# Performance work log

Measured on AMD Instinct MI355X. Metric: run time of the kernel, lower is better.

## Reference

```python
import jax, jax.numpy as jnp
import numpy as np

N, E, D = 100000, 640000, 128

def setup_inputs() -> dict:
    key = jax.random.key(0)
    ks = jax.random.split(key, 12)
    s = 1.0 / np.sqrt(D)
    sg = 1.0 / np.sqrt(2 * D)
    return {
        "nodes": jax.random.normal(ks[0], (N, D), jnp.float32),
        "globals_": jax.random.normal(ks[1], (1, D), jnp.float32),
        "senders": jax.random.randint(ks[2], (E,), 0, N, jnp.int32),
        "receivers": jax.random.randint(ks[3], (E,), 0, N, jnp.int32),
        "W1_w": jax.random.normal(ks[4], (D, D), jnp.float32) * s,
        "W1_b": jnp.zeros((D,), jnp.float32),
        "W2_w": jax.random.normal(ks[5], (D, D), jnp.float32) * s,
        "W2_b": jnp.zeros((D,), jnp.float32),
        "W3_w": jax.random.normal(ks[6], (D, D), jnp.float32) * s,
        "W3_b": jnp.zeros((D,), jnp.float32),
        "Wg_w": jax.random.normal(ks[7], (2 * D, D), jnp.float32) * sg,
        "Wg_b": jnp.zeros((D,), jnp.float32),
    }


def reference(nodes, globals_, senders, receivers,
              W1_w, W1_b, W2_w, W2_b, W3_w, W3_b, Wg_w, Wg_b):
    n = nodes.shape[0]
    # W1 skip-branch projection
    h = nodes @ W1_w + W1_b                              # [N, D]
    # GraphConvolution: W2 projection + symmetric-normalized sum aggregation
    conv = nodes @ W2_w + W2_b                           # [N, D]
    ones = jnp.ones(senders.shape, conv.dtype)
    send_deg = jax.ops.segment_sum(ones, senders, num_segments=n)
    recv_deg = jax.ops.segment_sum(ones, receivers, num_segments=n)
    conv = conv * jax.lax.rsqrt(jnp.maximum(send_deg, 1.0))[:, None]
    agg = jax.ops.segment_sum(conv[senders], receivers, num_segments=n)  # gather + scatter
    agg = agg * jax.lax.rsqrt(jnp.maximum(recv_deg, 1.0))[:, None]
    h = h + agg
    # global -> node broadcast (globals is not None)
    h = h + (globals_[0:1] @ W3_w + W3_b)
    h = jax.nn.relu(h)
    h = h + nodes                                        # residual
    # global update: aggregate nodes (sum over single graph) + gated residual
    an = jnp.sum(h, axis=0, keepdims=True)               # [1, D]
    g_new = globals_ + jax.nn.relu(jnp.concatenate([an, globals_], axis=-1) @ Wg_w + Wg_b)
    return h, g_new
```

## Files before the change

kernel.cpp:

```cpp
#include <hip/hip_runtime.h>

#define D 128
#define SCH 1024

typedef __attribute__((ext_vector_type(8))) short short8;
typedef __attribute__((ext_vector_type(4))) float floatx4;

__device__ inline void bf16split(float x, ushort& hi, ushort& lo) {
  unsigned u = __float_as_uint(x);
  unsigned rh = (u + 0x7FFFu + ((u >> 16) & 1u)) & 0xFFFF0000u;
  hi = (ushort)(rh >> 16);
  float fl = x - __uint_as_float(rh);
  unsigned ul = __float_as_uint(fl);
  lo = (ushort)((ul + 0x7FFFu + ((ul >> 16) & 1u)) >> 16);
}

__global__ void k_gproj(const float* __restrict__ g, const float* __restrict__ W3,
                        const float* __restrict__ b3, float* __restrict__ gvec,
                        float* __restrict__ an) {
  if (blockIdx.x == 1) {
    if (threadIdx.x < D) an[threadIdx.x] = 0.f;
    return;
  }
  __shared__ float part[256];
  const int j = threadIdx.x & 127, half = threadIdx.x >> 7;
  float acc = 0.f;
  for (int k = half * 64; k < half * 64 + 64; ++k)
    acc = fmaf(g[k], W3[k * D + j], acc);
  part[threadIdx.x] = acc;
  __syncthreads();
  if (threadIdx.x < D) gvec[j] = b3[j] + part[j] + part[j + 128];
}

__global__ void k_degrees(const int* __restrict__ snd, const int* __restrict__ rcv,
                          int* __restrict__ cs, int* __restrict__ cr, int E) {
  const int e = blockIdx.x * blockDim.x + threadIdx.x;
  if (e < E) {
    atomicAdd(cs + snd[e], 1);
    atomicAdd(cr + rcv[e], 1);
  }
}

__global__ void k_scanA(const int* __restrict__ cnt, int* __restrict__ bsum, int n) {
  __shared__ int red[4];
  const int t = threadIdx.x;
  const int base = blockIdx.x * SCH + t * 4;
  int4 v = make_int4(0, 0, 0, 0);
  if (base < n) v = *(const int4*)(cnt + base);
  int s = v.x + v.y + v.z + v.w;
#pragma unroll
  for (int o = 32; o > 0; o >>= 1) s += __shfl_down(s, o, 64);
  if ((t & 63) == 0) red[t >> 6] = s;
  __syncthreads();
  if (t == 0) bsum[blockIdx.x] = red[0] + red[1] + red[2] + red[3];
}

__global__ void k_scanB(const int* __restrict__ bsum, int* __restrict__ bbase, int nb) {
  __shared__ int sh[256];
  const int t = threadIdx.x;
  const int v = (t < nb) ? bsum[t] : 0;
  sh[t] = v;
  __syncthreads();
  for (int st = 1; st < 256; st <<= 1) {
    const int u = (t >= st) ? sh[t - st] : 0;
    __syncthreads();
    sh[t] += u;
    __syncthreads();
  }
  if (t < nb) bbase[t] = sh[t] - v;
}

__global__ void k_scanC(const int* __restrict__ cnt, const int* __restrict__ bbase,
                        int* __restrict__ off, int* __restrict__ cursor, int n) {
  __shared__ int sh[256];
  const int t = threadIdx.x;
  const int base = blockIdx.x * SCH + t * 4;
  int4 v = make_int4(0, 0, 0, 0);
  if (base < n) v = *(const int4*)(cnt + base);
  const int s = v.x + v.y + v.z + v.w;
  sh[t] = s;
  __syncthreads();
  for (int st = 1; st < 256; st <<= 1) {
    const int u = (t >= st) ? sh[t - st] : 0;
    __syncthreads();
    sh[t] += u;
    __syncthreads();
  }
  const int ex = sh[t] - s + bbase[blockIdx.x];
  if (base < n) {
    const int4 o = make_int4(ex, ex + v.x, ex + v.x + v.y, ex + v.x + v.y + v.z);
    *(int4*)(off + base) = o;
    *(int4*)(cursor + base) = o;
  }
}

__global__ void k_fill(const int* __restrict__ snd, const int* __restrict__ rcv,
                       int* __restrict__ cursor, int* __restrict__ srt, int E) {
  const int e = blockIdx.x * blockDim.x + threadIdx.x;
  if (e < E) {
    const int p = atomicAdd(cursor + rcv[e], 1);
    srt[p] = snd[e];
  }
}

__global__ void k_wsplit(const float* __restrict__ W1, const float* __restrict__ W2,
                         ushort* __restrict__ wt) {
  const int id = blockIdx.x * blockDim.x + threadIdx.x;
  const int mat = id >> 14;
  const int idx = id & 16383;
  const int k = idx >> 7;
  const int n = idx & 127;
  const float x = (mat ? W2 : W1)[k * D + n];
  ushort hi, lo;
  bf16split(x, hi, lo);
  wt[(size_t)mat * 32768 + (size_t)n * 128 + k] = hi;
  wt[(size_t)mat * 32768 + 16384 + (size_t)n * 128 + k] = lo;
}

__global__ __launch_bounds__(256, 3) void k_gemm(
    const float* __restrict__ A, const ushort* __restrict__ wt,
    const float* __restrict__ b1, const float* __restrict__ b2,
    const float* __restrict__ gvec, const int* __restrict__ cnt_send,
    float* __restrict__ outH, float* __restrict__ conv, int n) {
  __shared__ ushort Ah[64 * 40], Al[64 * 40], Wh[256 * 40], Wl[256 * 40];
  const int t = threadIdx.x;
  const int row0 = blockIdx.x * 64;
  const int lane = t & 63, w = t >> 6;
  const int m = lane & 15, quad = lane >> 4;

  floatx4 acc[4][4];
#pragma unroll
  for (int i = 0; i < 4; ++i)
#pragma unroll
    for (int j = 0; j < 4; ++j) acc[i][j] = (floatx4)0.f;

  const int arow = t >> 2, akl = (t & 3) * 8;
  const int wcol = t;
  const int wmat = wcol >> 7, wn = wcol & 127;

  for (int p = 0; p < 4; ++p) {
    {
      const int grow = row0 + arow;
      const bool ok = grow < n;
      const float* gp = A + (size_t)grow * D + p * 32 + akl;
      float4 v0 = make_float4(0.f, 0.f, 0.f, 0.f), v1 = v0;
      if (ok) {
        v0 = *(const float4*)gp;
        v1 = *(const float4*)(gp + 4);
      }
      ushort h0, l0, h1, l1, h2, l2, h3, l3;
      const int a = arow * 40 + akl;
      bf16split(v0.x, h0, l0); bf16split(v0.y, h1, l1);
      bf16split(v0.z, h2, l2); bf16split(v0.w, h3, l3);
      *(ushort4*)&Ah[a] = make_ushort4(h0, h1, h2, h3);
      *(ushort4*)&Al[a] = make_ushort4(l0, l1, l2, l3);
      bf16split(v1.x, h0, l0); bf16split(v1.y, h1, l1);
      bf16split(v1.z, h2, l2); bf16split(v1.w, h3, l3);
      *(ushort4*)&Ah[a + 4] = make_ushort4(h0, h1, h2, h3);
      *(ushort4*)&Al[a + 4] = make_ushort4(l0, l1, l2, l3);
    }
    {
      const ushort* gh = wt + (size_t)wmat * 32768 + (size_t)wn * 128 + p * 32;
      const ushort* gl = gh + 16384;
      const int a = wcol * 40;
#pragma unroll
      for (int c = 0; c < 4; ++c) {
        *(uint4*)&Wh[a + 8 * c] = *(const uint4*)(gh + 8 * c);
        *(uint4*)&Wl[a + 8 * c] = *(const uint4*)(gl + 8 * c);
      }
    }
    __syncthreads();
    short8 a_h[4], a_l[4];
#pragma unroll
    for (int i = 0; i < 4; ++i) {
      const int r = (i * 16 + m) * 40 + quad * 8;
      a_h[i] = *(const short8*)&Ah[r];
      a_l[i] = *(const short8*)&Al[r];
    }
#pragma unroll
    for (int j = 0; j < 4; ++j) {
      const int r = (w * 64 + j * 16 + m) * 40 + quad * 8;
      const short8 b_h = *(const short8*)&Wh[r];
      const short8 b_l = *(const short8*)&Wl[r];
#pragma unroll
      for (int i = 0; i < 4; ++i) {
        floatx4 c = acc[i][j];
        c = __builtin_amdgcn_mfma_f32_16x16x32_bf16(a_h[i], b_h, c, 0, 0, 0);
        c = __builtin_amdgcn_mfma_f32_16x16x32_bf16(a_h[i], b_l, c, 0, 0, 0);
        c = __builtin_amdgcn_mfma_f32_16x16x32_bf16(a_l[i], b_h, c, 0, 0, 0);
        acc[i][j] = c;
      }
    }
    __syncthreads();
  }

  if (w < 2) {
    float bb[4], gg[4];
#pragma unroll
    for (int j = 0; j < 4; ++j) {
      const int col = w * 64 + j * 16 + m;
      bb[j] = b1[col];
      gg[j] = gvec[col];
    }
#pragma unroll
    for (int i = 0; i < 4; ++i)
#pragma unroll
      for (int pp = 0; pp < 4; ++pp) {
        const int rg = row0 + i * 16 + quad * 4 + pp;
        if (rg >= n) continue;
#pragma unroll
        for (int j = 0; j < 4; ++j) {
          const int col = w * 64 + j * 16 + m;
          outH[(size_t)rg * D + col] = acc[i][j][pp] + bb[j] + gg[j];
        }
      }
  } else {
    float bb[4];
#pragma unroll
    for (int j = 0; j < 4; ++j) bb[j] = b2[(w - 2) * 64 + j * 16 + m];
#pragma unroll
    for (int i = 0; i < 4; ++i)
#pragma unroll
      for (int pp = 0; pp < 4; ++pp) {
        const int rg = row0 + i * 16 + quad * 4 + pp;
        if (rg >= n) continue;
        const float sc = rsqrtf(fmaxf((float)cnt_send[rg], 1.f));
#pragma unroll
        for (int j = 0; j < 4; ++j) {
          const int col = (w - 2) * 64 + j * 16 + m;
          conv[(size_t)rg * D + col] = (acc[i][j][pp] + bb[j]) * sc;
        }
      }
  }
}

__global__ __launch_bounds__(256) void k_agg_finalize(
    const float* __restrict__ conv, const int* __restrict__ off,
    const int* __restrict__ cnt_recv, const int* __restrict__ srt,
    const float* __restrict__ nodes, float* __restrict__ h,
    float* __restrict__ an, int n) {
  __shared__ float anl[8][D];
  const int hw = threadIdx.x >> 5;
  const int ln = threadIdx.x & 31;
  const int ghw = blockIdx.x * 8 + hw;
  const int nhw = gridDim.x * 8;
  const int c0 = ln * 4;

  float a0 = 0.f, a1 = 0.f, a2 = 0.f, a3 = 0.f;

  for (int r0 = ghw; r0 < n; r0 += 2 * nhw) {
    const int r1 = r0 + nhw;
    const bool has1 = r1 < n;
    const int dg0 = cnt_recv[r0];
    const int o0 = off[r0];
    const int dg1 = has1 ? cnt_recv[r1] : 0;
    const int o1 = has1 ? off[r1] : o0;

    int idx0[8], idx1[8];
    float mk0[8], mk1[8];
#pragma unroll
    for (int j = 0; j < 8; ++j) {
      const bool v0 = j < dg0;
      idx0[j] = srt[o0 + (v0 ? j : 0)];
      mk0[j] = v0 ? 1.f : 0.f;
      const bool v1 = j < dg1;
      idx1[j] = srt[o1 + (v1 ? j : 0)];
      mk1[j] = v1 ? 1.f : 0.f;
    }
    const float4 h10 = *(const float4*)(h + (size_t)r0 * D + c0);
    const float4 nd0 = *(const float4*)(nodes + (size_t)r0 * D + c0);
    float4 c0v[8], c1v[8];
#pragma unroll
    for (int j = 0; j < 8; ++j)
      c0v[j] = *(const float4*)(conv + (size_t)idx0[j] * D + c0);
#pragma unroll
    for (int j = 0; j < 8; ++j)
      c1v[j] = *(const float4*)(conv + (size_t)idx1[j] * D + c0);

    float sx0 = 0.f, sy0 = 0.f, sz0 = 0.f, sw0 = 0.f;
    float sx1 = 0.f, sy1 = 0.f, sz1 = 0.f, sw1 = 0.f;
#pragma unroll
    for (int j = 0; j < 8; ++j) {
      sx0 = fmaf(mk0[j], c0v[j].x, sx0);
      sy0 = fmaf(mk0[j], c0v[j].y, sy0);
      sz0 = fmaf(mk0[j], c0v[j].z, sz0);
      sw0 = fmaf(mk0[j], c0v[j].w, sw0);
      sx1 = fmaf(mk1[j], c1v[j].x, sx1);
      sy1 = fmaf(mk1[j], c1v[j].y, sy1);
      sz1 = fmaf(mk1[j], c1v[j].z, sz1);
      sw1 = fmaf(mk1[j], c1v[j].w, sw1);
    }
    for (int i = 8; i < dg0; ++i) {
      const int s = srt[o0 + i];
      const float4 c = *(const float4*)(conv + (size_t)s * D + c0);
      sx0 += c.x; sy0 += c.y; sz0 += c.z; sw0 += c.w;
    }
    for (int i = 8; i < dg1; ++i) {
      const int s = srt[o1 + i];
      const float4 c = *(const float4*)(conv + (size_t)s * D + c0);
      sx1 += c.x; sy1 += c.y; sz1 += c.z; sw1 += c.w;
    }

    {
      const float sc = rsqrtf(fmaxf((float)dg0, 1.f));
      const float x0 = fmaxf(h10.x + sx0 * sc, 0.f) + nd0.x;
      const float x1 = fmaxf(h10.y + sy0 * sc, 0.f) + nd0.y;
      const float x2 = fmaxf(h10.z + sz0 * sc, 0.f) + nd0.z;
      const float x3 = fmaxf(h10.w + sw0 * sc, 0.f) + nd0.w;
      *(float4*)(h + (size_t)r0 * D + c0) = make_float4(x0, x1, x2, x3);
      a0 += x0; a1 += x1; a2 += x2; a3 += x3;
    }
    if (has1) {
      const float4 h11 = *(const float4*)(h + (size_t)r1 * D + c0);
      const float4 nd1 = *(const float4*)(nodes + (size_t)r1 * D + c0);
      const float sc = rsqrtf(fmaxf((float)dg1, 1.f));
      const float x0 = fmaxf(h11.x + sx1 * sc, 0.f) + nd1.x;
      const float x1 = fmaxf(h11.y + sy1 * sc, 0.f) + nd1.y;
      const float x2 = fmaxf(h11.z + sz1 * sc, 0.f) + nd1.z;
      const float x3 = fmaxf(h11.w + sw1 * sc, 0.f) + nd1.w;
      *(float4*)(h + (size_t)r1 * D + c0) = make_float4(x0, x1, x2, x3);
      a0 += x0; a1 += x1; a2 += x2; a3 += x3;
    }
  }
  anl[hw][c0 + 0] = a0;
  anl[hw][c0 + 1] = a1;
  anl[hw][c0 + 2] = a2;
  anl[hw][c0 + 3] = a3;
  __syncthreads();
  if (threadIdx.x < D) {
    float s = 0.f;
#pragma unroll
    for (int k = 0; k < 8; ++k) s += anl[k][threadIdx.x];
    atomicAdd(an + threadIdx.x, s);
  }
}

__global__ void k_gupdate(const float* __restrict__ an, const float* __restrict__ g,
                          const float* __restrict__ Wg, const float* __restrict__ bg,
                          float* __restrict__ gout) {
  __shared__ float part[256];
  const int j = threadIdx.x & 127, half = threadIdx.x >> 7;
  float acc = 0.f;
  if (half == 0) {
    for (int k = 0; k < D; ++k) acc = fmaf(an[k], Wg[k * D + j], acc);
  } else {
    for (int k = 0; k < D; ++k) acc = fmaf(g[k], Wg[(D + k) * D + j], acc);
  }
  part[threadIdx.x] = acc;
  __syncthreads();
  if (threadIdx.x < D)
    gout[j] = g[j] + fmaxf(bg[j] + part[j] + part[j + 128], 0.f);
}

extern "C" void kernel_launch(void* const* d_in, const int* in_sizes, int n_in,
                              void* d_out, int out_size, void* d_ws, size_t ws_size,
                              hipStream_t stream) {
  const float* nodes = (const float*)d_in[0];
  const float* globals_ = (const float*)d_in[1];
  const int* senders = (const int*)d_in[2];
  const int* receivers = (const int*)d_in[3];
  const float* W1_w = (const float*)d_in[4];
  const float* W1_b = (const float*)d_in[5];
  const float* W2_w = (const float*)d_in[6];
  const float* W2_b = (const float*)d_in[7];
  const float* W3_w = (const float*)d_in[8];
  const float* W3_b = (const float*)d_in[9];
  const float* Wg_w = (const float*)d_in[10];
  const float* Wg_b = (const float*)d_in[11];
  const int N = in_sizes[0] / D;
  const int E = in_sizes[2];
  const int nb = (N + SCH - 1) / SCH;

  float* h = (float*)d_out;
  float* gout = h + (size_t)N * D;

  float* ws = (float*)d_ws;
  float* conv = ws;
  int* cnt_send = (int*)(ws + (size_t)N * D);
  int* cnt_recv = cnt_send + N;
  int* off = cnt_recv + N;
  int* cursor = off + N;
  int* srt = cursor + N;
  float* gvec = (float*)(srt + E);
  float* an = gvec + D;
  int* bsum = (int*)(an + D);
  int* bbase = bsum + 256;
  ushort* wt = (ushort*)cursor;

  (void)hipMemsetAsync(cnt_send, 0, 2 * (size_t)N * sizeof(int), stream);

  hipLaunchKernelGGL(k_gproj, dim3(2), dim3(256), 0, stream, globals_, W3_w, W3_b,
                     gvec, an);
  hipLaunchKernelGGL(k_degrees, dim3((E + 255) / 256), dim3(256), 0, stream,
                     senders, receivers, cnt_send, cnt_recv, E);
  hipLaunchKernelGGL(k_scanA, dim3(nb), dim3(256), 0, stream, cnt_recv, bsum, N);
  hipLaunchKernelGGL(k_scanB, dim3(1), dim3(256), 0, stream, bsum, bbase, nb);
  hipLaunchKernelGGL(k_scanC, dim3(nb), dim3(256), 0, stream, cnt_recv, bbase,
                     off, cursor, N);
  hipLaunchKernelGGL(k_fill, dim3((E + 255) / 256), dim3(256), 0, stream,
                     senders, receivers, cursor, srt, E);
  hipLaunchKernelGGL(k_wsplit, dim3(128), dim3(256), 0, stream, W1_w, W2_w, wt);
  hipLaunchKernelGGL(k_gemm, dim3((N + 63) / 64), dim3(256), 0, stream,
                     nodes, wt, W1_b, W2_b, gvec, cnt_send, h, conv, N);
  hipLaunchKernelGGL(k_agg_finalize, dim3(2048), dim3(256), 0, stream,
                     conv, off, cnt_recv, srt, nodes, h, an, N);
  hipLaunchKernelGGL(k_gupdate, dim3(1), dim3(256), 0, stream, an, globals_,
                     Wg_w, Wg_b, gout);
}
```

Before: 374.4 us.

## Aggregate raw nodes before W2 projection and fuse epilogue into GEMM

Reorders the graph convolution so neighbours' raw node features are aggregated first (with sender/receiver normalisation) into a bf16 hi/lo split buffer. A single GEMM then computes nodes@W1 + agg@W2 together with bias, relu, residual and the global-sum epilogue. This removes the separate conv write/read and the finalize pass over h. The scan becomes a single-pass decoupled lookback and the small kernels are merged, cutting launches. Risks include spin-waiting on inter-block ordering in the scan and a GEMM that now does twice the MFMA work per output column.

```diff
diff --git a/kernel.cpp b/kernel.cpp
--- a/kernel.cpp
+++ b/kernel.cpp
@@ -2,6 +2,7 @@
 
 #define D 128
 #define SCH 1024
+#define AGGB 2048
 
 typedef __attribute__((ext_vector_type(8))) short short8;
 typedef __attribute__((ext_vector_type(4))) float floatx4;
@@ -15,14 +16,19 @@
   lo = (ushort)((ul + 0x7FFFu + ((ul >> 16) & 1u)) >> 16);
 }
 
-__global__ void k_gproj(const float* __restrict__ g, const float* __restrict__ W3,
-                        const float* __restrict__ b3, float* __restrict__ gvec,
-                        float* __restrict__ an) {
-  if (blockIdx.x == 1) {
-    if (threadIdx.x < D) an[threadIdx.x] = 0.f;
+__global__ void k_front(const int* __restrict__ snd, const int* __restrict__ rcv,
+                        int* __restrict__ cs, int* __restrict__ cr, int E, int nbE,
+                        const float* __restrict__ g, const float* __restrict__ W3,
+                        const float* __restrict__ b3, float* __restrict__ gvec) {
+  __shared__ float part[256];
+  if ((int)blockIdx.x < nbE) {
+    const int e = blockIdx.x * 256 + threadIdx.x;
+    if (e < E) {
+      atomicAdd(cs + snd[e], 1);
+      atomicAdd(cr + rcv[e], 1);
+    }
     return;
   }
-  __shared__ float part[256];
   const int j = threadIdx.x & 127, half = threadIdx.x >> 7;
   float acc = 0.f;
   for (int k = half * 64; k < half * 64 + 64; ++k)
@@ -32,49 +38,12 @@
   if (threadIdx.x < D) gvec[j] = b3[j] + part[j] + part[j + 128];
 }
 
-__global__ void k_degrees(const int* __restrict__ snd, const int* __restrict__ rcv,
-                          int* __restrict__ cs, int* __restrict__ cr, int E) {
-  const int e = blockIdx.x * blockDim.x + threadIdx.x;
-  if (e < E) {
-    atomicAdd(cs + snd[e], 1);
-    atomicAdd(cr + rcv[e], 1);
-  }
-}
-
-__global__ void k_scanA(const int* __restrict__ cnt, int* __restrict__ bsum, int n) {
+__global__ void k_scan(const int* __restrict__ cnt, int* __restrict__ bsum,
+                       int* __restrict__ off, int* __restrict__ cursor, int n) {
+  __shared__ int sh[256];
   __shared__ int red[4];
-  const int t = threadIdx.x;
-  const int base = blockIdx.x * SCH + t * 4;
-  int4 v = make_int4(0, 0, 0, 0);
-  if (base < n) v = *(const int4*)(cnt + base);
-  int s = v.x + v.y + v.z + v.w;
-#pragma unroll
-  for (int o = 32; o > 0; o >>= 1) s += __shfl_down(s, o, 64);
-  if ((t & 63) == 0) red[t >> 6] = s;
-  __syncthreads();
-  if (t == 0) bsum[blockIdx.x] = red[0] + red[1] + red[2] + red[3];
-}
-
-__global__ void k_scanB(const int* __restrict__ bsum, int* __restrict__ bbase, int nb) {
-  __shared__ int sh[256];
-  const int t = threadIdx.x;
-  const int v = (t < nb) ? bsum[t] : 0;
-  sh[t] = v;
-  __syncthreads();
-  for (int st = 1; st < 256; st <<= 1) {
-    const int u = (t >= st) ? sh[t - st] : 0;
-    __syncthreads();
-    sh[t] += u;
-    __syncthreads();
-  }
-  if (t < nb) bbase[t] = sh[t] - v;
-}
-
-__global__ void k_scanC(const int* __restrict__ cnt, const int* __restrict__ bbase,
-                        int* __restrict__ off, int* __restrict__ cursor, int n) {
-  __shared__ int sh[256];
-  const int t = threadIdx.x;
-  const int base = blockIdx.x * SCH + t * 4;
+  const int t = threadIdx.x, b = blockIdx.x;
+  const int base = b * SCH + t * 4;
   int4 v = make_int4(0, 0, 0, 0);
   if (base < n) v = *(const int4*)(cnt + base);
   const int s = v.x + v.y + v.z + v.w;
@@ -86,11 +55,26 @@
     sh[t] += u;
     __syncthreads();
   }
-  const int ex = sh[t] - s + bbase[blockIdx.x];
+  if (t == 255) atomicExch(bsum + b, sh[255] + 1);
+  int pre = 0;
+  if (t < b) {
+    int x = atomicAdd(bsum + t, 0);
+    while (x == 0) {
+      __builtin_amdgcn_s_sleep(1);
+      x = atomicAdd(bsum + t, 0);
+    }
+    pre = x - 1;
+  }
+#pragma unroll
+  for (int o = 32; o > 0; o >>= 1) pre += __shfl_down(pre, o, 64);
+  if ((t & 63) == 0) red[t >> 6] = pre;
+  __syncthreads();
+  const int gbase = red[0] + red[1] + red[2] + red[3];
+  const int ex = sh[t] - s + gbase;
   if (base < n) {
-    const int4 o = make_int4(ex, ex + v.x, ex + v.x + v.y, ex + v.x + v.y + v.z);
-    *(int4*)(off + base) = o;
-    *(int4*)(cursor + base) = o;
+    const int4 o4 = make_int4(ex, ex + v.x, ex + v.x + v.y, ex + v.x + v.y + v.z);
+    *(int4*)(off + base) = o4;
+    *(int4*)(cursor + base) = o4;
   }
 }
 
@@ -103,45 +87,142 @@
   }
 }
 
-__global__ void k_wsplit(const float* __restrict__ W1, const float* __restrict__ W2,
-                         ushort* __restrict__ wt) {
-  const int id = blockIdx.x * blockDim.x + threadIdx.x;
-  const int mat = id >> 14;
-  const int idx = id & 16383;
-  const int k = idx >> 7;
-  const int n = idx & 127;
-  const float x = (mat ? W2 : W1)[k * D + n];
-  ushort hi, lo;
-  bf16split(x, hi, lo);
-  wt[(size_t)mat * 32768 + (size_t)n * 128 + k] = hi;
-  wt[(size_t)mat * 32768 + 16384 + (size_t)n * 128 + k] = lo;
-}
-
-__global__ __launch_bounds__(256, 3) void k_gemm(
-    const float* __restrict__ A, const ushort* __restrict__ wt,
+__global__ __launch_bounds__(256) void k_agg(
+    const float* __restrict__ nodes, const int* __restrict__ off,
+    int* __restrict__ cnt_recv, const int* __restrict__ cnt_send,
+    const int* __restrict__ srt, ushort* __restrict__ yh,
+    ushort* __restrict__ yl, int n, const float* __restrict__ W1,
+    const float* __restrict__ W2, ushort* __restrict__ wt) {
+  if ((int)blockIdx.x >= AGGB) {
+    const int id = ((int)blockIdx.x - AGGB) * 256 + threadIdx.x;
+    const int mat = id >> 14, idx = id & 16383;
+    const int k = idx >> 7, nn = idx & 127;
+    const float x = (mat ? W2 : W1)[k * D + nn];
+    ushort hi, lo;
+    bf16split(x, hi, lo);
+    wt[(size_t)mat * 32768 + (size_t)nn * 128 + k] = hi;
+    wt[(size_t)mat * 32768 + 16384 + (size_t)nn * 128 + k] = lo;
+    return;
+  }
+  float* cf = (float*)cnt_recv;
+  const int hw = threadIdx.x >> 5, ln = threadIdx.x & 31;
+  const int ghw = blockIdx.x * 8 + hw;
+  const int nhw = AGGB * 8;
+  const int c0 = ln * 4;
+
+  for (int r0 = ghw; r0 < n; r0 += 2 * nhw) {
+    const int r1 = r0 + nhw;
+    const bool has1 = r1 < n;
+    const int dg0 = cnt_recv[r0];
+    const int o0 = off[r0];
+    const int dg1 = has1 ? cnt_recv[r1] : 0;
+    const int o1 = has1 ? off[r1] : o0;
+    const int safe0 = (dg0 > 0) ? o0 : 0;
+    const int safe1 = (dg1 > 0) ? o1 : 0;
+
+    int idx0[8], idx1[8];
+#pragma unroll
+    for (int j = 0; j < 8; ++j) {
+      idx0[j] = srt[safe0 + (j < dg0 ? j : 0)];
+      idx1[j] = srt[safe1 + (j < dg1 ? j : 0)];
+    }
+    float4 g0[8], g1[8];
+#pragma unroll
+    for (int j = 0; j < 8; ++j)
+      g0[j] = *(const float4*)(nodes + (size_t)idx0[j] * D + c0);
+#pragma unroll
+    for (int j = 0; j < 8; ++j)
+      g1[j] = *(const float4*)(nodes + (size_t)idx1[j] * D + c0);
+    float rs0[8], rs1[8];
+#pragma unroll
+    for (int j = 0; j < 8; ++j) {
+      rs0[j] = (j < dg0) ? rsqrtf(fmaxf((float)cnt_send[idx0[j]], 1.f)) : 0.f;
+      rs1[j] = (j < dg1) ? rsqrtf(fmaxf((float)cnt_send[idx1[j]], 1.f)) : 0.f;
+    }
+
+    float sx0 = 0.f, sy0 = 0.f, sz0 = 0.f, sw0 = 0.f, cs0 = 0.f;
+    float sx1 = 0.f, sy1 = 0.f, sz1 = 0.f, sw1 = 0.f, cs1 = 0.f;
+#pragma unroll
+    for (int j = 0; j < 8; ++j) {
+      sx0 = fmaf(rs0[j], g0[j].x, sx0);
+      sy0 = fmaf(rs0[j], g0[j].y, sy0);
+      sz0 = fmaf(rs0[j], g0[j].z, sz0);
+      sw0 = fmaf(rs0[j], g0[j].w, sw0);
+      cs0 += rs0[j];
+      sx1 = fmaf(rs1[j], g1[j].x, sx1);
+      sy1 = fmaf(rs1[j], g1[j].y, sy1);
+      sz1 = fmaf(rs1[j], g1[j].z, sz1);
+      sw1 = fmaf(rs1[j], g1[j].w, sw1);
+      cs1 += rs1[j];
+    }
+    for (int i = 8; i < dg0; ++i) {
+      const int s = srt[o0 + i];
+      const float r = rsqrtf(fmaxf((float)cnt_send[s], 1.f));
+      const float4 c = *(const float4*)(nodes + (size_t)s * D + c0);
+      sx0 = fmaf(r, c.x, sx0); sy0 = fmaf(r, c.y, sy0);
+      sz0 = fmaf(r, c.z, sz0); sw0 = fmaf(r, c.w, sw0);
+      cs0 += r;
+    }
+    for (int i = 8; i < dg1; ++i) {
+      const int s = srt[o1 + i];
+      const float r = rsqrtf(fmaxf((float)cnt_send[s], 1.f));
+      const float4 c = *(const float4*)(nodes + (size_t)s * D + c0);
+      sx1 = fmaf(r, c.x, sx1); sy1 = fmaf(r, c.y, sy1);
+      sz1 = fmaf(r, c.z, sz1); sw1 = fmaf(r, c.w, sw1);
+      cs1 += r;
+    }
+
+    {
+      const float rr = rsqrtf(fmaxf((float)dg0, 1.f));
+      ushort h0, l0, h1, l1, h2, l2, h3, l3;
+      bf16split(sx0 * rr, h0, l0);
+      bf16split(sy0 * rr, h1, l1);
+      bf16split(sz0 * rr, h2, l2);
+      bf16split(sw0 * rr, h3, l3);
+      *(ushort4*)(yh + (size_t)r0 * D + c0) = make_ushort4(h0, h1, h2, h3);
+      *(ushort4*)(yl + (size_t)r0 * D + c0) = make_ushort4(l0, l1, l2, l3);
+      if (ln == 0) cf[r0] = rr * cs0;
+    }
+    if (has1) {
+      const float rr = rsqrtf(fmaxf((float)dg1, 1.f));
+      ushort h0, l0, h1, l1, h2, l2, h3, l3;
+      bf16split(sx1 * rr, h0, l0);
+      bf16split(sy1 * rr, h1, l1);
+      bf16split(sz1 * rr, h2, l2);
+      bf16split(sw1 * rr, h3, l3);
+      *(ushort4*)(yh + (size_t)r1 * D + c0) = make_ushort4(h0, h1, h2, h3);
+      *(ushort4*)(yl + (size_t)r1 * D + c0) = make_ushort4(l0, l1, l2, l3);
+      if (ln == 0) cf[r1] = rr * cs1;
+    }
+  }
+}
+
+__global__ __launch_bounds__(256, 2) void k_gemm(
+    const float* __restrict__ A, const ushort* __restrict__ yh,
+    const ushort* __restrict__ yl, const ushort* __restrict__ wt,
     const float* __restrict__ b1, const float* __restrict__ b2,
-    const float* __restrict__ gvec, const int* __restrict__ cnt_send,
-    float* __restrict__ outH, float* __restrict__ conv, int n) {
-  __shared__ ushort Ah[64 * 40], Al[64 * 40], Wh[256 * 40], Wl[256 * 40];
+    const float* __restrict__ gvec, const float* __restrict__ cf,
+    float* __restrict__ outH, float* __restrict__ an, int n) {
+  __shared__ ushort A1h[64 * 40], A1l[64 * 40], A2h[64 * 40], A2l[64 * 40];
+  __shared__ ushort Wh[256 * 40], Wl[256 * 40];
   const int t = threadIdx.x;
   const int row0 = blockIdx.x * 64;
   const int lane = t & 63, w = t >> 6;
   const int m = lane & 15, quad = lane >> 4;
 
-  floatx4 acc[4][4];
+  floatx4 acc[4][2];
 #pragma unroll
   for (int i = 0; i < 4; ++i)
 #pragma unroll
-    for (int j = 0; j < 4; ++j) acc[i][j] = (floatx4)0.f;
+    for (int j = 0; j < 2; ++j) acc[i][j] = (floatx4)0.f;
 
   const int arow = t >> 2, akl = (t & 3) * 8;
-  const int wcol = t;
-  const int wmat = wcol >> 7, wn = wcol & 127;
+  const int wcol = t, wmat = wcol >> 7, wn = wcol & 127;
+  const int grow = row0 + arow;
+  const bool ok = grow < n;
 
   for (int p = 0; p < 4; ++p) {
     {
-      const int grow = row0 + arow;
-      const bool ok = grow < n;
       const float* gp = A + (size_t)grow * D + p * 32 + akl;
       float4 v0 = make_float4(0.f, 0.f, 0.f, 0.f), v1 = v0;
       if (ok) {
@@ -152,12 +233,17 @@
       const int a = arow * 40 + akl;
       bf16split(v0.x, h0, l0); bf16split(v0.y, h1, l1);
       bf16split(v0.z, h2, l2); bf16split(v0.w, h3, l3);
-      *(ushort4*)&Ah[a] = make_ushort4(h0, h1, h2, h3);
-      *(ushort4*)&Al[a] = make_ushort4(l0, l1, l2, l3);
+      *(ushort4*)&A1h[a] = make_ushort4(h0, h1, h2, h3);
+      *(ushort4*)&A1l[a] = make_ushort4(l0, l1, l2, l3);
       bf16split(v1.x, h0, l0); bf16split(v1.y, h1, l1);
       bf16split(v1.z, h2, l2); bf16split(v1.w, h3, l3);
-      *(ushort4*)&Ah[a + 4] = make_ushort4(h0, h1, h2, h3);
-      *(ushort4*)&Al[a + 4] = make_ushort4(l0, l1, l2, l3);
+      *(ushort4*)&A1h[a + 4] = make_ushort4(h0, h1, h2, h3);
+      *(ushort4*)&A1l[a + 4] = make_ushort4(l0, l1, l2, l3);
+    }
+    if (ok) {
+      const int a = arow * 40 + akl;
+      *(uint4*)&A2h[a] = *(const uint4*)(yh + (size_t)grow * D + p * 32 + akl);
+      *(uint4*)&A2l[a] = *(const uint4*)(yl + (size_t)grow * D + p * 32 + akl);
     }
     {
       const ushort* gh = wt + (size_t)wmat * 32768 + (size_t)wn * 128 + p * 32;
@@ -170,168 +256,68 @@
       }
     }
     __syncthreads();
-    short8 a_h[4], a_l[4];
+    short8 a1h[4], a1l[4], a2h[4], a2l[4];
 #pragma unroll
     for (int i = 0; i < 4; ++i) {
       const int r = (i * 16 + m) * 40 + quad * 8;
-      a_h[i] = *(const short8*)&Ah[r];
-      a_l[i] = *(const short8*)&Al[r];
-    }
-#pragma unroll
-    for (int j = 0; j < 4; ++j) {
-      const int r = (w * 64 + j * 16 + m) * 40 + quad * 8;
-      const short8 b_h = *(const short8*)&Wh[r];
-      const short8 b_l = *(const short8*)&Wl[r];
+      a1h[i] = *(const short8*)&A1h[r];
+      a1l[i] = *(const short8*)&A1l[r];
+      a2h[i] = *(const short8*)&A2h[r];
+      a2l[i] = *(const short8*)&A2l[r];
+    }
+#pragma unroll
+    for (int j = 0; j < 2; ++j) {
+      const int r1 = (w * 32 + j * 16 + m) * 40 + quad * 8;
+      const int r2 = (128 + w * 32 + j * 16 + m) * 40 + quad * 8;
+      const short8 w1h = *(const short8*)&Wh[r1];
+      const short8 w1l = *(const short8*)&Wl[r1];
+      const short8 w2h = *(const short8*)&Wh[r2];
+      const short8 w2l = *(const short8*)&Wl[r2];
 #pragma unroll
       for (int i = 0; i < 4; ++i) {
         floatx4 c = acc[i][j];
-        c = __builtin_amdgcn_mfma_f32_16x16x32_bf16(a_h[i], b_h, c, 0, 0, 0);
-        c = __builtin_amdgcn_mfma_f32_16x16x32_bf16(a_h[i], b_l, c, 0, 0, 0);
-        c = __builtin_amdgcn_mfma_f32_16x16x32_bf16(a_l[i], b_h, c, 0, 0, 0);
+        c = __builtin_amdgcn_mfma_f32_16x16x32_bf16(a1h[i], w1h, c, 0, 0, 0);
+        c = __builtin_amdgcn_mfma_f32_16x16x32_bf16(a1h[i], w1l, c, 0, 0, 0);
+        c = __builtin_amdgcn_mfma_f32_16x16x32_bf16(a1l[i], w1h, c, 0, 0, 0);
+        c = __builtin_amdgcn_mfma_f32_16x16x32_bf16(a2h[i], w2h, c, 0, 0, 0);
+        c = __builtin_amdgcn_mfma_f32_16x16x32_bf16(a2h[i], w2l, c, 0, 0, 0);
+        c = __builtin_amdgcn_mfma_f32_16x16x32_bf16(a2l[i], w2h, c, 0, 0, 0);
         acc[i][j] = c;
       }
     }
     __syncthreads();
   }
 
-  if (w < 2) {
-    float bb[4], gg[4];
-#pragma unroll
-    for (int j = 0; j < 4; ++j) {
-      const int col = w * 64 + j * 16 + m;
-      bb[j] = b1[col];
-      gg[j] = gvec[col];
-    }
-#pragma unroll
-    for (int i = 0; i < 4; ++i)
-#pragma unroll
-      for (int pp = 0; pp < 4; ++pp) {
-        const int rg = row0 + i * 16 + quad * 4 + pp;
-        if (rg >= n) continue;
-#pragma unroll
-        for (int j = 0; j < 4; ++j) {
-          const int col = w * 64 + j * 16 + m;
-          outH[(size_t)rg * D + col] = acc[i][j][pp] + bb[j] + gg[j];
-        }
+  float bb[2], b2c[2];
+#pragma unroll
+  for (int j = 0; j < 2; ++j) {
+    const int col = w * 32 + j * 16 + m;
+    bb[j] = b1[col] + gvec[col];
+    b2c[j] = b2[col];
+  }
+  float asum[2] = {0.f, 0.f};
+#pragma unroll
+  for (int i = 0; i < 4; ++i)
+#pragma unroll
+    for (int pp = 0; pp < 4; ++pp) {
+      const int rg = row0 + i * 16 + quad * 4 + pp;
+      if (rg >= n) continue;
+      const float crv = cf[rg];
+#pragma unroll
+      for (int j = 0; j < 2; ++j) {
+        const int col = w * 32 + j * 16 + m;
+        float v = acc[i][j][pp] + bb[j] + crv * b2c[j];
+        v = fmaxf(v, 0.f) + A[(size_t)rg * D + col];
+        outH[(size_t)rg * D + col] = v;
+        asum[j] += v;
       }
-  } else {
-    float bb[4];
-#pragma unroll
-    for (int j = 0; j < 4; ++j) bb[j] = b2[(w - 2) * 64 + j * 16 + m];
-#pragma unroll
-    for (int i = 0; i < 4; ++i)
-#pragma unroll
-      for (int pp = 0; pp < 4; ++pp) {
-        const int rg = row0 + i * 16 + quad * 4 + pp;
-        if (rg >= n) continue;
-        const float sc = rsqrtf(fmaxf((float)cnt_send[rg], 1.f));
-#pragma unroll
-        for (int j = 0; j < 4; ++j) {
-          const int col = (w - 2) * 64 + j * 16 + m;
-          conv[(size_t)rg * D + col] = (acc[i][j][pp] + bb[j]) * sc;
-        }
-      }
-  }
-}
-
-__global__ __launch_bounds__(256) void k_agg_finalize(
-    const float* __restrict__ conv, const int* __restrict__ off,
-    const int* __restrict__ cnt_recv, const int* __restrict__ srt,
-    const float* __restrict__ nodes, float* __restrict__ h,
-    float* __restrict__ an, int n) {
-  __shared__ float anl[8][D];
-  const int hw = threadIdx.x >> 5;
-  const int ln = threadIdx.x & 31;
-  const int ghw = blockIdx.x * 8 + hw;
-  const int nhw = gridDim.x * 8;
-  const int c0 = ln * 4;
-
-  float a0 = 0.f, a1 = 0.f, a2 = 0.f, a3 = 0.f;
-
-  for (int r0 = ghw; r0 < n; r0 += 2 * nhw) {
-    const int r1 = r0 + nhw;
-    const bool has1 = r1 < n;
-    const int dg0 = cnt_recv[r0];
-    const int o0 = off[r0];
-    const int dg1 = has1 ? cnt_recv[r1] : 0;
-    const int o1 = has1 ? off[r1] : o0;
-
-    int idx0[8], idx1[8];
-    float mk0[8], mk1[8];
-#pragma unroll
-    for (int j = 0; j < 8; ++j) {
-      const bool v0 = j < dg0;
-      idx0[j] = srt[o0 + (v0 ? j : 0)];
-      mk0[j] = v0 ? 1.f : 0.f;
-      const bool v1 = j < dg1;
-      idx1[j] = srt[o1 + (v1 ? j : 0)];
-      mk1[j] = v1 ? 1.f : 0.f;
-    }
-    const float4 h10 = *(const float4*)(h + (size_t)r0 * D + c0);
-    const float4 nd0 = *(const float4*)(nodes + (size_t)r0 * D + c0);
-    float4 c0v[8], c1v[8];
-#pragma unroll
-    for (int j = 0; j < 8; ++j)
-      c0v[j] = *(const float4*)(conv + (size_t)idx0[j] * D + c0);
-#pragma unroll
-    for (int j = 0; j < 8; ++j)
-      c1v[j] = *(const float4*)(conv + (size_t)idx1[j] * D + c0);
-
-    float sx0 = 0.f, sy0 = 0.f, sz0 = 0.f, sw0 = 0.f;
-    float sx1 = 0.f, sy1 = 0.f, sz1 = 0.f, sw1 = 0.f;
-#pragma unroll
-    for (int j = 0; j < 8; ++j) {
-      sx0 = fmaf(mk0[j], c0v[j].x, sx0);
-      sy0 = fmaf(mk0[j], c0v[j].y, sy0);
-      sz0 = fmaf(mk0[j], c0v[j].z, sz0);
-      sw0 = fmaf(mk0[j], c0v[j].w, sw0);
-      sx1 = fmaf(mk1[j], c1v[j].x, sx1);
-      sy1 = fmaf(mk1[j], c1v[j].y, sy1);
-      sz1 = fmaf(mk1[j], c1v[j].z, sz1);
-      sw1 = fmaf(mk1[j], c1v[j].w, sw1);
-    }
-    for (int i = 8; i < dg0; ++i) {
-      const int s = srt[o0 + i];
-      const float4 c = *(const float4*)(conv + (size_t)s * D + c0);
-      sx0 += c.x; sy0 += c.y; sz0 += c.z; sw0 += c.w;
-    }
-    for (int i = 8; i < dg1; ++i) {
-      const int s = srt[o1 + i];
-      const float4 c = *(const float4*)(conv + (size_t)s * D + c0);
-      sx1 += c.x; sy1 += c.y; sz1 += c.z; sw1 += c.w;
-    }
-
-    {
-      const float sc = rsqrtf(fmaxf((float)dg0, 1.f));
-      const float x0 = fmaxf(h10.x + sx0 * sc, 0.f) + nd0.x;
-      const float x1 = fmaxf(h10.y + sy0 * sc, 0.f) + nd0.y;
-      const float x2 = fmaxf(h10.z + sz0 * sc, 0.f) + nd0.z;
-      const float x3 = fmaxf(h10.w + sw0 * sc, 0.f) + nd0.w;
-      *(float4*)(h + (size_t)r0 * D + c0) = make_float4(x0, x1, x2, x3);
-      a0 += x0; a1 += x1; a2 += x2; a3 += x3;
-    }
-    if (has1) {
-      const float4 h11 = *(const float4*)(h + (size_t)r1 * D + c0);
-      const float4 nd1 = *(const float4*)(nodes + (size_t)r1 * D + c0);
-      const float sc = rsqrtf(fmaxf((float)dg1, 1.f));
-      const float x0 = fmaxf(h11.x + sx1 * sc, 0.f) + nd1.x;
-      const float x1 = fmaxf(h11.y + sy1 * sc, 0.f) + nd1.y;
-      const float x2 = fmaxf(h11.z + sz1 * sc, 0.f) + nd1.z;
-      const float x3 = fmaxf(h11.w + sw1 * sc, 0.f) + nd1.w;
-      *(float4*)(h + (size_t)r1 * D + c0) = make_float4(x0, x1, x2, x3);
-      a0 += x0; a1 += x1; a2 += x2; a3 += x3;
-    }
-  }
-  anl[hw][c0 + 0] = a0;
-  anl[hw][c0 + 1] = a1;
-  anl[hw][c0 + 2] = a2;
-  anl[hw][c0 + 3] = a3;
-  __syncthreads();
-  if (threadIdx.x < D) {
-    float s = 0.f;
-#pragma unroll
-    for (int k = 0; k < 8; ++k) s += anl[k][threadIdx.x];
-    atomicAdd(an + threadIdx.x, s);
+    }
+#pragma unroll
+  for (int j = 0; j < 2; ++j) {
+    float v = asum[j];
+    v += __shfl_xor(v, 16);
+    v += __shfl_xor(v, 32);
+    if (lane < 16) atomicAdd(an + w * 32 + j * 16 + m, v);
   }
 }
 
@@ -370,40 +356,39 @@
   const int N = in_sizes[0] / D;
   const int E = in_sizes[2];
   const int nb = (N + SCH - 1) / SCH;
+  const int nbE = (E + 255) / 256;
 
   float* h = (float*)d_out;
   float* gout = h + (size_t)N * D;
 
   float* ws = (float*)d_ws;
-  float* conv = ws;
-  int* cnt_send = (int*)(ws + (size_t)N * D);
+  ushort* yh = (ushort*)ws;
+  ushort* yl = yh + (size_t)N * D;
+  int* cnt_send = (int*)(yl + (size_t)N * D);
   int* cnt_recv = cnt_send + N;
-  int* off = cnt_recv + N;
+  int* bsum = cnt_recv + N;
+  float* an = (float*)(bsum + 256);
+  int* off = (int*)(an + D);
   int* cursor = off + N;
   int* srt = cursor + N;
   float* gvec = (float*)(srt + E);
-  float* an = gvec + D;
-  int* bsum = (int*)(an + D);
-  int* bbase = bsum + 256;
   ushort* wt = (ushort*)cursor;
 
-  (void)hipMemsetAsync(cnt_send, 0, 2 * (size_t)N * sizeof(int), stream);
-
-  hipLaunchKernelGGL(k_gproj, dim3(2), dim3(256), 0, stream, globals_, W3_w, W3_b,
-                     gvec, an);
-  hipLaunchKernelGGL(k_degrees, dim3((E + 255) / 256), dim3(256), 0, stream,
-                     senders, receivers, cnt_send, cnt_recv, E);
-  hipLaunchKernelGGL(k_scanA, dim3(nb), dim3(256), 0, stream, cnt_recv, bsum, N);
-  hipLaunchKernelGGL(k_scanB, dim3(1), dim3(256), 0, stream, bsum, bbase, nb);
-  hipLaunchKernelGGL(k_scanC, dim3(nb), dim3(256), 0, stream, cnt_recv, bbase,
-                     off, cursor, N);
-  hipLaunchKernelGGL(k_fill, dim3((E + 255) / 256), dim3(256), 0, stream,
+  (void)hipMemsetAsync(cnt_send, 0, (size_t)(2 * N + 256 + D) * sizeof(int), stream);
+
+  hipLaunchKernelGGL(k_front, dim3(nbE + 1), dim3(256), 0, stream,
+                     senders, receivers, cnt_send, cnt_recv, E, nbE,
+                     globals_, W3_w, W3_b, gvec);
+  hipLaunchKernelGGL(k_scan, dim3(nb), dim3(256), 0, stream,
+                     cnt_recv, bsum, off, cursor, N);
+  hipLaunchKernelGGL(k_fill, dim3(nbE), dim3(256), 0, stream,
                      senders, receivers, cursor, srt, E);
-  hipLaunchKernelGGL(k_wsplit, dim3(128), dim3(256), 0, stream, W1_w, W2_w, wt);
+  hipLaunchKernelGGL(k_agg, dim3(AGGB + 128), dim3(256), 0, stream,
+                     nodes, off, cnt_recv, cnt_send, srt, yh, yl, N,
+                     W1_w, W2_w, wt);
   hipLaunchKernelGGL(k_gemm, dim3((N + 63) / 64), dim3(256), 0, stream,
-                     nodes, wt, W1_b, W2_b, gvec, cnt_send, h, conv, N);
-  hipLaunchKernelGGL(k_agg_finalize, dim3(2048), dim3(256), 0, stream,
-                     conv, off, cnt_recv, srt, nodes, h, an, N);
+                     nodes, yh, yl, wt, W1_b, W2_b, gvec,
+                     (const float*)cnt_recv, h, an, N);
   hipLaunchKernelGGL(k_gupdate, dim3(1), dim3(256), 0, stream, an, globals_,
                      Wg_w, Wg_b, gout);
 }
```

Result: faster. 362.9 us (-3.1%).
